# Performance work log

Measured on AMD Instinct MI355X. Metric: run time of the kernel, lower is better.

The kernel has to match this reference:

```python
import jax, jax.numpy as jnp
import numpy as np

B, T, I, H, L = 32, 512, 256, 512, 4


def setup_inputs() -> dict:
    key = jax.random.key(0)
    ks = jax.random.split(key, 20)
    s = 0.01
    d = {"inputs": jax.random.normal(ks[0], (B, T, I), jnp.float32)}
    # layer-0 input->hidden weights (input dim I)
    for n, k in zip(["Wxi0", "Wxf0", "Wxo0", "Wxc0"], ks[1:5]):
        d[n] = jax.random.normal(k, (I, H), jnp.float32) * s
    # layers 1..L-1 input->hidden weights (input dim H), stacked
    for n, k in zip(["Wxi", "Wxf", "Wxo", "Wxc"], ks[5:9]):
        d[n] = jax.random.normal(k, (L - 1, H, H), jnp.float32) * s
    # hidden->hidden weights, stacked over layers
    for n, k in zip(["Whi", "Whf", "Who", "Whc"], ks[9:13]):
        d[n] = jax.random.normal(k, (L, H, H), jnp.float32) * s
    for n in ["bi", "bf", "bo", "bc"]:
        d[n] = jnp.zeros((L, H), jnp.float32)
    return d


def _lstm(inputs, Wxi0, Wxf0, Wxo0, Wxc0, Wxi, Wxf, Wxo, Wxc,
          Whi, Whf, Who, Whc, bi, bf, bo, bc):
    b, t, _ = inputs.shape
    h0 = jnp.zeros((L, b, H), inputs.dtype)
    c0 = jnp.zeros((L, b, H), inputs.dtype)

    def step(carry, x_t):
        h, c = carry  # each [L, B, H]
        new_h, new_c = [], []
        inp = x_t
        for l in range(L):
            if l == 0:
                wxi, wxf, wxo, wxc = Wxi0, Wxf0, Wxo0, Wxc0
            else:
                wxi, wxf, wxo, wxc = Wxi[l - 1], Wxf[l - 1], Wxo[l - 1], Wxc[l - 1]
            it = jax.nn.sigmoid(h[l] @ Whi[l] + inp @ wxi + bi[l])
            ft = jax.nn.sigmoid(h[l] @ Whf[l] + inp @ wxf + bf[l])
            ot = jax.nn.sigmoid(h[l] @ Who[l] + inp @ wxo + bo[l])
            ct_tilde = jnp.tanh(h[l] @ Whc[l] + inp @ wxc + bc[l])
            ct = ft * c[l] + it * ct_tilde
            ht = ot * jnp.tanh(ct)
            new_h.append(ht)
            new_c.append(ct)
            inp = ht
        return (jnp.stack(new_h), jnp.stack(new_c)), new_h[-1]

    _, outs = jax.lax.scan(step, (h0, c0), jnp.swapaxes(inputs, 0, 1))
    return jnp.swapaxes(outs, 0, 1)  # [B, T, H]


def reference(inputs, Wxi0, Wxf0, Wxo0, Wxc0, Wxi, Wxf, Wxo, Wxc,
              Whi, Whf, Who, Whc, bi, bf, bo, bc):
    return _lstm(inputs, Wxi0, Wxf0, Wxo0, Wxc0, Wxi, Wxf, Wxo, Wxc,
                 Whi, Whf, Who, Whc, bi, bf, bo, bc)
```

## Files before the change

kernel.cpp:

```cpp
#include <hip/hip_runtime.h>


constexpr int Bv = 32;
constexpr int Tv = 512;
constexpr int Iv = 256;
constexpr int Hv = 512;
constexpr int LAYv = 4;
constexpr int SLICES = 64;
constexpr int THREADS = 256;
constexpr int NKK = 32;
constexpr int WTAB = 2 * NKK * 64 * 8;
constexpr int PRE = 32 * 33;
constexpr unsigned SMEM_BYTES = WTAB * 2 * 2 + 2 * PRE * 4;

typedef short sfrag __attribute__((ext_vector_type(8)));
typedef float facc  __attribute__((ext_vector_type(4)));
typedef float f32x4 __attribute__((ext_vector_type(4)));

struct Params {
  const float *x;
  const float *Wx0i, *Wx0f, *Wx0o, *Wx0c;
  const float *Wxi, *Wxf, *Wxo, *Wxc;
  const float *Whi, *Whf, *Who, *Whc;
  const float *bi, *bf, *bo, *bc;
  float *out;
  unsigned short *hbuf;
  unsigned char *flags;
  int dmask;
};

__device__ __forceinline__ unsigned short f2bf(float f) {
  unsigned int u = __builtin_bit_cast(unsigned int, f);
  u += 0x7FFFu + ((u >> 16) & 1u);
  return (unsigned short)(u >> 16);
}
__device__ __forceinline__ float bf2f(unsigned short s) {
  unsigned int u = ((unsigned int)s) << 16;
  return __builtin_bit_cast(float, u);
}

__device__ __forceinline__ int ld_flagb_bypass(const unsigned char *p) {
  int v;
  asm volatile("global_load_ubyte %0, %1, off sc0 sc1\n\t"
               "s_waitcnt vmcnt(0)"
               : "=v"(v) : "v"(p) : "memory");
  return v;
}
__device__ __forceinline__ void st_flagb_bypass(unsigned char *p) {
  asm volatile("global_store_byte %0, %1, off sc0 sc1" ::"v"(p), "v"(1)
               : "memory");
}
__device__ __forceinline__ void st_short_bypass(unsigned short *p, unsigned short v) {
  asm volatile("global_store_short %0, %1, off sc0 sc1" ::"v"(p), "v"(v)
               : "memory");
}
__device__ __forceinline__ void poll_pair(const unsigned char *f0) {
  while (ld_flagb_bypass(f0) == 0) __builtin_amdgcn_s_sleep(1);
  while (ld_flagb_bypass(f0 + 64) == 0) __builtin_amdgcn_s_sleep(1);
}

__global__ void __launch_bounds__(THREADS, 1) lstm_pipeline(Params p) {
  const int wg = blockIdx.x;
  const int l = wg >> 6;
  const int slice = wg & 63;
  const int tid = threadIdx.x;
  const int lane = tid & 63;
  const int w = tid >> 6;
  const int mt = w & 1;
  const int nt = w >> 1;

  extern __shared__ char smem[];
  unsigned short *wlds_hi = (unsigned short *)smem;
  unsigned short *wlds_lo = wlds_hi + WTAB;
  float *pre0 = (float *)(smem + (size_t)WTAB * 2 * 2);

  const float *Wh[4] = {p.Whi + (size_t)l * Hv * Hv, p.Whf + (size_t)l * Hv * Hv,
                        p.Who + (size_t)l * Hv * Hv, p.Whc + (size_t)l * Hv * Hv};
  const float *Wx[4];
  if (l == 0) { Wx[0] = p.Wx0i; Wx[1] = p.Wx0f; Wx[2] = p.Wx0o; Wx[3] = p.Wx0c; }
  else {
    size_t o = (size_t)(l - 1) * Hv * Hv;
    Wx[0] = p.Wxi + o; Wx[1] = p.Wxf + o; Wx[2] = p.Wxo + o; Wx[3] = p.Wxc + o;
  }
  const int kx_max = (l == 0) ? Iv : Hv;

  for (int idx = tid; idx < 2 * NKK * 64; idx += THREADS) {
    int lanei = idx & 63;
    int kk = (idx >> 6) & (NKK - 1);
    int nti = idx >> 11;
    int kbase = kk * 32 + (lanei >> 4) * 8;
    int n = nti * 16 + (lanei & 15);
    int jj = n >> 2, g = n & 3;
    int col = slice * 8 + jj;
    sfrag vh, vl;
#pragma unroll
    for (int j = 0; j < 8; ++j) {
      int k = kbase + j;
      float wv;
      if (k < Hv) wv = Wh[g][(size_t)k * Hv + col];
      else {
        int kx = k - Hv;
        wv = (kx < kx_max) ? Wx[g][(size_t)kx * Hv + col] : 0.f;
      }
      unsigned short h16 = f2bf(wv);
      vh[j] = (short)h16;
      vl[j] = (short)f2bf(wv - bf2f(h16));
    }
    *(sfrag *)&wlds_hi[(size_t)idx * 8] = vh;
    *(sfrag *)&wlds_lo[(size_t)idx * 8] = vl;
  }

  const int bm = tid >> 3;
  const int um = tid & 7;
  const int jg = slice * 8 + um;
  const float bia_i = p.bi[l * Hv + jg];
  const float bia_f = p.bf[l * Hv + jg];
  const float bia_o = p.bo[l * Hv + jg];
  const float bia_c = p.bc[l * Hv + jg];
  float cstate = 0.f;

  __syncthreads();

  const int m = mt * 16 + (lane & 15);
  const int kgrp = lane >> 4;
  unsigned char *flags = p.flags;
  unsigned short *hbuf = p.hbuf;
  const int dmask = p.dmask;

#define MFMA_BURST(A, KKB, CNT)                                                \
  {                                                                            \
    _Pragma("unroll") for (int j = 0; j < (CNT); ++j) {                        \
      sfrag bh =                                                               \
          *(const sfrag *)&wlds_hi[(size_t)((nt * NKK + (KKB) + j) * 64 + lane) * 8]; \
      sfrag bl =                                                               \
          *(const sfrag *)&wlds_lo[(size_t)((nt * NKK + (KKB) + j) * 64 + lane) * 8]; \
      acc0 = __builtin_amdgcn_mfma_f32_16x16x32_bf16(A[j], bh, acc0, 0, 0, 0); \
      acc1 = __builtin_amdgcn_mfma_f32_16x16x32_bf16(A[j], bl, acc1, 0, 0, 0); \
    }                                                                          \
  }

  for (int t = 0; t < Tv; ++t) {
    facc acc0 = {0.f, 0.f, 0.f, 0.f};
    facc acc1 = {0.f, 0.f, 0.f, 0.f};

    if (l == 0) {
      const float *xbp = p.x + ((size_t)m * Tv + t) * Iv + kgrp * 8;
#pragma unroll
      for (int kk = 0; kk < 8; ++kk) {
        f32x4 lo = *(const f32x4 *)(xbp + kk * 32);
        f32x4 hi = *(const f32x4 *)(xbp + kk * 32 + 4);
        sfrag ax;
#pragma unroll
        for (int j = 0; j < 4; ++j) {
          ax[j] = (short)f2bf(lo[j]);
          ax[4 + j] = (short)f2bf(hi[j]);
        }
        sfrag bh = *(const sfrag *)&wlds_hi[(size_t)((nt * NKK + 16 + kk) * 64 + lane) * 8];
        sfrag bl = *(const sfrag *)&wlds_lo[(size_t)((nt * NKK + 16 + kk) * 64 + lane) * 8];
        acc0 = __builtin_amdgcn_mfma_f32_16x16x32_bf16(ax, bh, acc0, 0, 0, 0);
        acc1 = __builtin_amdgcn_mfma_f32_16x16x32_bf16(ax, bl, acc1, 0, 0, 0);
      }
    } else {
      poll_pair(flags + ((size_t)(t * LAYv + (l - 1))) * 256 + (2 * mt) * 64 + lane);
      const unsigned short *hin =
          hbuf + ((size_t)(((t + 1) & dmask) * LAYv + (l - 1)) * Bv * Hv) +
          (size_t)m * Hv;
      sfrag ain[16];
#pragma unroll
      for (int kk = 0; kk < 16; ++kk)
        ain[kk] = *(const sfrag *)(hin + kk * 32 + kgrp * 8);
      MFMA_BURST(ain, 16, 16)
    }

    if (t > 0) {
      poll_pair(flags + ((size_t)((t - 1) * LAYv + l)) * 256 + (2 * mt) * 64 + lane);
      const unsigned short *hrec =
          hbuf + ((size_t)((t & dmask) * LAYv + l) * Bv * Hv) + (size_t)m * Hv;
      sfrag arec[16];
#pragma unroll
      for (int kk = 0; kk < 16; ++kk)
        arec[kk] = *(const sfrag *)(hrec + kk * 32 + kgrp * 8);
      MFMA_BURST(arec, 0, 16)
    }

    float *pa = pre0 + (t & 1) * PRE;
    {
      int row = mt * 16 + kgrp * 4;
      int coln = nt * 16 + (lane & 15);
#pragma unroll
      for (int r = 0; r < 4; ++r)
        pa[(row + r) * 33 + coln] = acc0[r] + acc1[r];
    }
    __syncthreads();

    float pi = pa[bm * 33 + um * 4 + 0] + bia_i;
    float pf = pa[bm * 33 + um * 4 + 1] + bia_f;
    float po = pa[bm * 33 + um * 4 + 2] + bia_o;
    float pc = pa[bm * 33 + um * 4 + 3] + bia_c;
    float gi = 1.f / (1.f + __expf(-pi));
    float gf = 1.f / (1.f + __expf(-pf));
    float go = 1.f / (1.f + __expf(-po));
    float gc = tanhf(pc);
    cstate = gf * cstate + gi * gc;
    float hval = go * tanhf(cstate);

    st_short_bypass(
        &hbuf[((size_t)(((t + 1) & dmask) * LAYv + l) * Bv * Hv) +
              (size_t)bm * Hv + jg],
        f2bf(hval));
    asm volatile("s_waitcnt vmcnt(0)" ::: "memory");
    if (lane == 0)
      st_flagb_bypass(flags + ((size_t)(t * LAYv + l)) * 256 + w * 64 + slice);

    if (l == LAYv - 1)
      p.out[((size_t)bm * Tv + t) * Hv + jg] = hval;
  }
#undef MFMA_BURST
}

extern "C" void kernel_launch(void *const *d_in, const int *in_sizes, int n_in,
                              void *d_out, int out_size, void *d_ws, size_t ws_size,
                              hipStream_t stream) {
  Params prm;
  prm.x = (const float *)d_in[0];
  prm.Wx0i = (const float *)d_in[1];
  prm.Wx0f = (const float *)d_in[2];
  prm.Wx0o = (const float *)d_in[3];
  prm.Wx0c = (const float *)d_in[4];
  prm.Wxi = (const float *)d_in[5];
  prm.Wxf = (const float *)d_in[6];
  prm.Wxo = (const float *)d_in[7];
  prm.Wxc = (const float *)d_in[8];
  prm.Whi = (const float *)d_in[9];
  prm.Whf = (const float *)d_in[10];
  prm.Who = (const float *)d_in[11];
  prm.Whc = (const float *)d_in[12];
  prm.bi = (const float *)d_in[13];
  prm.bf = (const float *)d_in[14];
  prm.bo = (const float *)d_in[15];
  prm.bc = (const float *)d_in[16];
  prm.out = (float *)d_out;

  size_t slot_bytes = (size_t)LAYv * Bv * Hv * sizeof(unsigned short);
  size_t fbytes = (size_t)Tv * LAYv * 4 * SLICES;
  size_t hslots = 512;
  if (ws_size < hslots * slot_bytes + fbytes) {
    hslots = 256;
    if (ws_size < hslots * slot_bytes + fbytes) return;
  }
  prm.dmask = (int)hslots - 1;
  prm.hbuf = (unsigned short *)d_ws;
  prm.flags = (unsigned char *)d_ws + hslots * slot_bytes;

  hipMemsetAsync(prm.flags, 0, fbytes, stream);

  hipFuncSetAttribute(reinterpret_cast<const void *>(lstm_pipeline),
                      hipFuncAttributeMaxDynamicSharedMemorySize, (int)SMEM_BYTES);

  hipLaunchKernelGGL(lstm_pipeline, dim3(LAYv * SLICES), dim3(THREADS),
                     SMEM_BYTES, stream, prm);
}
```

Baseline: 3.522 ms.

## Make each wave finish its own gates and drop the block barrier

Each wave now writes its 16x16 MFMA tile to a private LDS scratch and applies the LSTM gate math itself on 16 lanes, using 4 units per lane. This removes the per-timestep __syncthreads. The h output is stored as a single 8-byte bypass write per row, and output rows are written as float4. Flags are rearranged so a consumer waits for both producer waves with one 16-bit poll instead of two byte polls, which shortens the inter-workgroup dependency chain on the recurrent critical path. In exchange, only 16 of 64 lanes do the nonlinear math, so that part is more serialized.

```diff
diff --git a/kernel.cpp b/kernel.cpp
--- a/kernel.cpp
+++ b/kernel.cpp
@@ -10,10 +10,12 @@
 constexpr int THREADS = 256;
 constexpr int NKK = 32;
 constexpr int WTAB = 2 * NKK * 64 * 8;
-constexpr int PRE = 32 * 33;
-constexpr unsigned SMEM_BYTES = WTAB * 2 * 2 + 2 * PRE * 4;
+constexpr int SCR_STRIDE = 20;
+constexpr unsigned SMEM_BYTES = WTAB * 2 * 2 + 4 * 16 * SCR_STRIDE * 4;
 
 typedef short sfrag __attribute__((ext_vector_type(8)));
+typedef short short4v __attribute__((ext_vector_type(4)));
+typedef int   i32x2 __attribute__((ext_vector_type(2)));
 typedef float facc  __attribute__((ext_vector_type(4)));
 typedef float f32x4 __attribute__((ext_vector_type(4)));
 
@@ -39,9 +41,9 @@
   return __builtin_bit_cast(float, u);
 }
 
-__device__ __forceinline__ int ld_flagb_bypass(const unsigned char *p) {
+__device__ __forceinline__ int ld_flag_ushort_bypass(const unsigned char *p) {
   int v;
-  asm volatile("global_load_ubyte %0, %1, off sc0 sc1\n\t"
+  asm volatile("global_load_ushort %0, %1, off sc0 sc1\n\t"
                "s_waitcnt vmcnt(0)"
                : "=v"(v) : "v"(p) : "memory");
   return v;
@@ -50,13 +52,12 @@
   asm volatile("global_store_byte %0, %1, off sc0 sc1" ::"v"(p), "v"(1)
                : "memory");
 }
-__device__ __forceinline__ void st_short_bypass(unsigned short *p, unsigned short v) {
-  asm volatile("global_store_short %0, %1, off sc0 sc1" ::"v"(p), "v"(v)
+__device__ __forceinline__ void st_8b_bypass(unsigned short *p, i32x2 v) {
+  asm volatile("global_store_dwordx2 %0, %1, off sc0 sc1" ::"v"(p), "v"(v)
                : "memory");
 }
-__device__ __forceinline__ void poll_pair(const unsigned char *f0) {
-  while (ld_flagb_bypass(f0) == 0) __builtin_amdgcn_s_sleep(1);
-  while (ld_flagb_bypass(f0 + 64) == 0) __builtin_amdgcn_s_sleep(1);
+__device__ __forceinline__ void poll_line(const unsigned char *base) {
+  while (ld_flag_ushort_bypass(base) != 0x0101) __builtin_amdgcn_s_sleep(1);
 }
 
 __global__ void __launch_bounds__(THREADS, 1) lstm_pipeline(Params p) {
@@ -72,7 +73,8 @@
   extern __shared__ char smem[];
   unsigned short *wlds_hi = (unsigned short *)smem;
   unsigned short *wlds_lo = wlds_hi + WTAB;
-  float *pre0 = (float *)(smem + (size_t)WTAB * 2 * 2);
+  float *scratch = (float *)(smem + (size_t)WTAB * 2 * 2) +
+                   (size_t)w * 16 * SCR_STRIDE;
 
   const float *Wh[4] = {p.Whi + (size_t)l * Hv * Hv, p.Whf + (size_t)l * Hv * Hv,
                         p.Who + (size_t)l * Hv * Hv, p.Whc + (size_t)l * Hv * Hv};
@@ -110,14 +112,12 @@
     *(sfrag *)&wlds_lo[(size_t)idx * 8] = vl;
   }
 
-  const int bm = tid >> 3;
-  const int um = tid & 7;
-  const int jg = slice * 8 + um;
-  const float bia_i = p.bi[l * Hv + jg];
-  const float bia_f = p.bf[l * Hv + jg];
-  const float bia_o = p.bo[l * Hv + jg];
-  const float bia_c = p.bc[l * Hv + jg];
-  float cstate = 0.f;
+  const int ubase = slice * 8 + nt * 4;
+  f32x4 bi4 = *(const f32x4 *)&p.bi[l * Hv + ubase];
+  f32x4 bf4 = *(const f32x4 *)&p.bf[l * Hv + ubase];
+  f32x4 bo4 = *(const f32x4 *)&p.bo[l * Hv + ubase];
+  f32x4 bc4 = *(const f32x4 *)&p.bc[l * Hv + ubase];
+  float cst[4] = {0.f, 0.f, 0.f, 0.f};
 
   __syncthreads();
 
@@ -161,7 +161,7 @@
         acc1 = __builtin_amdgcn_mfma_f32_16x16x32_bf16(ax, bl, acc1, 0, 0, 0);
       }
     } else {
-      poll_pair(flags + ((size_t)(t * LAYv + (l - 1))) * 256 + (2 * mt) * 64 + lane);
+      poll_line(flags + ((size_t)(t * LAYv + (l - 1)) * 2 + mt) * 128 + lane * 2);
       const unsigned short *hin =
           hbuf + ((size_t)(((t + 1) & dmask) * LAYv + (l - 1)) * Bv * Hv) +
           (size_t)m * Hv;
@@ -173,7 +173,7 @@
     }
 
     if (t > 0) {
-      poll_pair(flags + ((size_t)((t - 1) * LAYv + l)) * 256 + (2 * mt) * 64 + lane);
+      poll_line(flags + ((size_t)((t - 1) * LAYv + l) * 2 + mt) * 128 + lane * 2);
       const unsigned short *hrec =
           hbuf + ((size_t)((t & dmask) * LAYv + l) * Bv * Hv) + (size_t)m * Hv;
       sfrag arec[16];
@@ -183,37 +183,47 @@
       MFMA_BURST(arec, 0, 16)
     }
 
-    float *pa = pre0 + (t & 1) * PRE;
     {
-      int row = mt * 16 + kgrp * 4;
-      int coln = nt * 16 + (lane & 15);
+      int rl = (lane >> 4) * 4;
+      int cl = lane & 15;
 #pragma unroll
       for (int r = 0; r < 4; ++r)
-        pa[(row + r) * 33 + coln] = acc0[r] + acc1[r];
-    }
-    __syncthreads();
-
-    float pi = pa[bm * 33 + um * 4 + 0] + bia_i;
-    float pf = pa[bm * 33 + um * 4 + 1] + bia_f;
-    float po = pa[bm * 33 + um * 4 + 2] + bia_o;
-    float pc = pa[bm * 33 + um * 4 + 3] + bia_c;
-    float gi = 1.f / (1.f + __expf(-pi));
-    float gf = 1.f / (1.f + __expf(-pf));
-    float go = 1.f / (1.f + __expf(-po));
-    float gc = tanhf(pc);
-    cstate = gf * cstate + gi * gc;
-    float hval = go * tanhf(cstate);
-
-    st_short_bypass(
-        &hbuf[((size_t)(((t + 1) & dmask) * LAYv + l) * Bv * Hv) +
-              (size_t)bm * Hv + jg],
-        f2bf(hval));
-    asm volatile("s_waitcnt vmcnt(0)" ::: "memory");
-    if (lane == 0)
-      st_flagb_bypass(flags + ((size_t)(t * LAYv + l)) * 256 + w * 64 + slice);
-
-    if (l == LAYv - 1)
-      p.out[((size_t)bm * Tv + t) * Hv + jg] = hval;
+        scratch[(rl + r) * SCR_STRIDE + cl] = acc0[r] + acc1[r];
+    }
+    if (lane < 16) {
+      int row = mt * 16 + lane;
+      f32x4 q0 = *(const f32x4 *)&scratch[lane * SCR_STRIDE + 0];
+      f32x4 q1 = *(const f32x4 *)&scratch[lane * SCR_STRIDE + 4];
+      f32x4 q2 = *(const f32x4 *)&scratch[lane * SCR_STRIDE + 8];
+      f32x4 q3 = *(const f32x4 *)&scratch[lane * SCR_STRIDE + 12];
+      f32x4 qs[4] = {q0, q1, q2, q3};
+      short4v sh;
+      f32x4 ov;
+#pragma unroll
+      for (int u = 0; u < 4; ++u) {
+        float pi = qs[u][0] + bi4[u];
+        float pf = qs[u][1] + bf4[u];
+        float po = qs[u][2] + bo4[u];
+        float pc = qs[u][3] + bc4[u];
+        float gi = 1.f / (1.f + __expf(-pi));
+        float gf = 1.f / (1.f + __expf(-pf));
+        float go = 1.f / (1.f + __expf(-po));
+        float gc = tanhf(pc);
+        cst[u] = gf * cst[u] + gi * gc;
+        float hval = go * tanhf(cst[u]);
+        sh[u] = (short)f2bf(hval);
+        ov[u] = hval;
+      }
+      st_8b_bypass(&hbuf[((size_t)(((t + 1) & dmask) * LAYv + l) * Bv * Hv) +
+                         (size_t)row * Hv + ubase],
+                   __builtin_bit_cast(i32x2, sh));
+      asm volatile("s_waitcnt vmcnt(0)" ::: "memory");
+      if (lane == 0)
+        st_flagb_bypass(flags + ((size_t)(t * LAYv + l) * 2 + mt) * 128 +
+                        slice * 2 + nt);
+      if (l == LAYv - 1)
+        *(f32x4 *)&p.out[((size_t)row * Tv + t) * Hv + ubase] = ov;
+    }
   }
 #undef MFMA_BURST
 }
@@ -242,7 +252,7 @@
   prm.out = (float *)d_out;
 
   size_t slot_bytes = (size_t)LAYv * Bv * Hv * sizeof(unsigned short);
-  size_t fbytes = (size_t)Tv * LAYv * 4 * SLICES;
+  size_t fbytes = (size_t)Tv * LAYv * 2 * 128;
   size_t hslots = 512;
   if (ws_size < hslots * slot_bytes + fbytes) {
     hslots = 256;
```

New measurement: 3.714 ms. 5.4% more time.
